# Kernel tuning notes

Measured on AMD Instinct MI355X. Metric: run time of the kernel, lower is better.

## Reference

```python
import jax, jax.numpy as jnp
import numpy as np

D_MODEL = 256
N_HEADS = 8
D_K = D_MODEL // N_HEADS
FFN_DIM = 1024
LN_EPS = 1e-5


def _layernorm(x, g, b):
    mu = jnp.mean(x, axis=-1, keepdims=True)
    var = jnp.var(x, axis=-1, keepdims=True)
    return (x - mu) * jax.lax.rsqrt(var + LN_EPS) * g + b


def setup_inputs() -> dict:
    key = jax.random.key(0)
    ks = jax.random.split(key, 16)
    B, Q, K = 2, 2048, 64
    s = 1.0 / np.sqrt(D_MODEL)
    inp = {
        "target_queries": jax.random.normal(ks[0], (B, Q, D_MODEL), jnp.float32),
        "sampled_features": jax.random.normal(ks[1], (B, Q, K, D_MODEL), jnp.float32),
        "Wq": jax.random.normal(ks[2], (D_MODEL, D_MODEL), jnp.float32) * s,
        "bq": jnp.zeros((D_MODEL,), jnp.float32),
        "Wk": jax.random.normal(ks[3], (D_MODEL, D_MODEL), jnp.float32) * s,
        "bk": jnp.zeros((D_MODEL,), jnp.float32),
        "Wv": jax.random.normal(ks[4], (D_MODEL, D_MODEL), jnp.float32) * s,
        "bv": jnp.zeros((D_MODEL,), jnp.float32),
        "Wo": jax.random.normal(ks[5], (D_MODEL, D_MODEL), jnp.float32) * s,
        "bo": jnp.zeros((D_MODEL,), jnp.float32),
        "g1": jnp.ones((D_MODEL,), jnp.float32),
        "beta1": jnp.zeros((D_MODEL,), jnp.float32),
        "g2": jnp.ones((D_MODEL,), jnp.float32),
        "beta2": jnp.zeros((D_MODEL,), jnp.float32),
        "W1": jax.random.normal(ks[6], (D_MODEL, FFN_DIM), jnp.float32) * s,
        "b1": jnp.zeros((FFN_DIM,), jnp.float32),
        "W2": jax.random.normal(ks[7], (FFN_DIM, D_MODEL), jnp.float32) * (1.0 / np.sqrt(FFN_DIM)),
        "b2": jnp.zeros((D_MODEL,), jnp.float32),
    }
    return inp


def reference(target_queries, sampled_features, Wq, bq, Wk, bk, Wv, bv, Wo, bo,
              g1, beta1, g2, beta2, W1, b1, W2, b2):
    B, Q, C = target_queries.shape
    K = sampled_features.shape[2]
    H, Dk = N_HEADS, D_K

    # pre-norm + projections (dropout is identity at eval)
    qn = _layernorm(target_queries, g1, beta1)
    q = (qn @ Wq + bq).reshape(B, Q, H, Dk).transpose(0, 2, 1, 3)            # bhqd
    k = (sampled_features @ Wk + bk).reshape(B, Q, K, H, Dk).transpose(0, 3, 1, 2, 4)  # bhqkd
    v = (sampled_features @ Wv + bv).reshape(B, Q, K, H, Dk).transpose(0, 3, 1, 2, 4)  # bhqkd

    # per-query gathered K/V attention
    scores = jnp.einsum('bhqd,bhqkd->bhqk', q, k) / np.sqrt(Dk).astype(np.float32)
    attn_weights = jax.nn.softmax(scores, axis=-1)                            # (B,H,Q,K)
    attn_out = jnp.einsum('bhqk,bhqkd->bhqd', attn_weights, v)
    attn_out = attn_out.transpose(0, 2, 1, 3).reshape(B, Q, C)
    attn_out = attn_out @ Wo + bo

    x = target_queries + attn_out

    # FFN with pre-norm residual (exact erf GELU, as torch default)
    h = _layernorm(x, g2, beta2)
    h = jax.nn.gelu(h @ W1 + b1, approximate=False) @ W2 + b2
    out = x + h
    return out, attn_weights
```

## Files before the change

kernel.cpp:

```cpp
#include <hip/hip_runtime.h>
#include <math.h>

#define QTOT 2048

using bf16x8 = __attribute__((ext_vector_type(8))) short;
using f32x4  = __attribute__((ext_vector_type(4))) float;

static __device__ __forceinline__ short f2bf(float f) {
    union { float f; unsigned u; } v; v.f = f;
    unsigned r = v.u + 0x7fffu + ((v.u >> 16) & 1u);
    return (short)(r >> 16);
}
static __device__ __forceinline__ unsigned cvt_pk(float a, float b) {
    unsigned r;
    asm("v_cvt_pk_bf16_f32 %0, %1, %2" : "=v"(r) : "v"(a), "v"(b));
    return r;
}
static __device__ __forceinline__ bf16x8 pack8(float a0, float a1, float a2, float a3,
                                               float a4, float a5, float a6, float a7) {
    union { unsigned u[4]; bf16x8 v; } z;
    z.u[0] = cvt_pk(a0, a1); z.u[1] = cvt_pk(a2, a3);
    z.u[2] = cvt_pk(a4, a5); z.u[3] = cvt_pk(a6, a7);
    return z.v;
}

__global__ void wconv(const float* __restrict__ Wq, const float* __restrict__ Wk,
                      const float* __restrict__ Wo, const float* __restrict__ Wv,
                      const float* __restrict__ W1, const float* __restrict__ W2,
                      short* __restrict__ WqP, short* __restrict__ WkP,
                      short* __restrict__ WoP, short* __restrict__ WvP,
                      short* __restrict__ W1P, short* __restrict__ W2P) {
    int b = blockIdx.x, t = threadIdx.x;
    const float* W; short* P; int N, KK, ci; bool tr = false;
    if (b < 32)       { W = Wq; P = WqP; N = 256;  KK = 8;  ci = b * 256 + t; }
    else if (b < 64)  { W = Wk; P = WkP; N = 256;  KK = 8;  ci = (b - 32) * 256 + t; tr = true; }
    else if (b < 96)  { W = Wo; P = WoP; N = 256;  KK = 8;  ci = (b - 64) * 256 + t; }
    else if (b < 128) { W = Wv; P = WvP; N = 256;  KK = 8;  ci = (b - 96) * 256 + t; }
    else if (b < 256) { W = W1; P = W1P; N = 1024; KK = 8;  ci = (b - 128) * 256 + t; }
    else              { W = W2; P = W2P; N = 256;  KK = 32; ci = (b - 256) * 256 + t; }
    int cb = ci / (KK * 64);
    int rem = ci - cb * (KK * 64);
    int kk = rem >> 6, l = rem & 63;
    int lr = l & 15, lg = l >> 4;
    int n = cb * 16 + lr, k0 = kk * 32 + lg * 8;
    short pk[8];
    if (!tr) {
#pragma unroll
        for (int e = 0; e < 8; ++e) pk[e] = f2bf(W[(size_t)(k0 + e) * N + n]);
    } else {
#pragma unroll
        for (int e = 0; e < 8; ++e) pk[e] = f2bf(W[(size_t)n * 256 + (k0 + e)]);
    }
    *reinterpret_cast<bf16x8*>(P + (size_t)ci * 8) = *reinterpret_cast<bf16x8*>(pk);
}

__global__ void ln1z(const float* __restrict__ tq, const short* __restrict__ WqP,
                     const float* __restrict__ bq, const float* __restrict__ g1,
                     const float* __restrict__ be1, const short* __restrict__ WkP,
                     const float* __restrict__ bk, short* __restrict__ zf,
                     float* __restrict__ sbg) {
    __shared__ float xs[8 * 260];
    __shared__ float qs[8 * 260];
    __shared__ short zst[8 * 2048];
    int r0 = blockIdx.x * 8, t = threadIdx.x;
    int w = t >> 6, l = t & 63, lr = l & 15, lg = l >> 4;
#pragma unroll
    for (int it = 0; it < 8; ++it) xs[it * 260 + t] = tq[(size_t)(r0 + it) * 256 + t];
    __syncthreads();
#pragma unroll
    for (int i = 0; i < 2; ++i) {
        int r = w * 2 + i;
        float s = 0.f, s2 = 0.f;
        for (int j = l; j < 256; j += 64) { float x = xs[r * 260 + j]; s += x; s2 += x * x; }
#pragma unroll
        for (int m = 1; m < 64; m <<= 1) { s += __shfl_xor(s, m); s2 += __shfl_xor(s2, m); }
        float mu = s * (1.f / 256.f);
        float var = s2 * (1.f / 256.f) - mu * mu;
        float rstd = rsqrtf(var + 1e-5f);
        for (int j = l; j < 256; j += 64)
            xs[r * 260 + j] = (xs[r * 260 + j] - mu) * rstd * g1[j] + be1[j];
    }
    __syncthreads();
    f32x4 cq[4];
#pragma unroll
    for (int ni = 0; ni < 4; ++ni) cq[ni] = (f32x4){0.f, 0.f, 0.f, 0.f};
#pragma unroll
    for (int kk = 0; kk < 8; ++kk) {
        bf16x8 af = {0, 0, 0, 0, 0, 0, 0, 0};
        if (lr < 8) {
            const float* xp = &xs[lr * 260 + kk * 32 + lg * 8];
            af = pack8(xp[0], xp[1], xp[2], xp[3], xp[4], xp[5], xp[6], xp[7]);
        }
#pragma unroll
        for (int ni = 0; ni < 4; ++ni) {
            bf16x8 bf = *reinterpret_cast<const bf16x8*>(WqP + ((size_t)((w * 4 + ni) * 8 + kk) * 64 + l) * 8);
            cq[ni] = __builtin_amdgcn_mfma_f32_16x16x32_bf16(af, bf, cq[ni], 0, 0, 0);
        }
    }
    if (lg < 2) {
#pragma unroll
        for (int ni = 0; ni < 4; ++ni)
#pragma unroll
            for (int r = 0; r < 4; ++r) {
                int row = lg * 4 + r, col = (w * 4 + ni) * 16 + lr;
                qs[row * 260 + col] = cq[ni][r] + bq[col];
            }
    }
    __syncthreads();
    if (t < 64) {
        int r = t >> 3, h = t & 7;
        float s = 0.f;
        for (int d = 0; d < 32; ++d) s += qs[r * 260 + h * 32 + d] * bk[h * 32 + d];
        sbg[(size_t)(r0 + r) * 8 + h] = s;
    }
    f32x4 cz[4][4];
#pragma unroll
    for (int mi = 0; mi < 4; ++mi)
#pragma unroll
        for (int ni = 0; ni < 4; ++ni) cz[mi][ni] = (f32x4){0.f, 0.f, 0.f, 0.f};
#pragma unroll
    for (int kk = 0; kk < 8; ++kk) {
        bf16x8 am[4];
#pragma unroll
        for (int mi = 0; mi < 4; ++mi) {
            bf16x8 z = {0, 0, 0, 0, 0, 0, 0, 0};
            if ((lr & 7) == kk) {
                int rr = mi * 2 + (lr >> 3);
                const float* qp = &qs[rr * 260 + kk * 32 + lg * 8];
                z = pack8(qp[0], qp[1], qp[2], qp[3], qp[4], qp[5], qp[6], qp[7]);
            }
            am[mi] = z;
        }
#pragma unroll
        for (int ni = 0; ni < 4; ++ni) {
            bf16x8 bf = *reinterpret_cast<const bf16x8*>(WkP + ((size_t)((w * 4 + ni) * 8 + kk) * 64 + l) * 8);
#pragma unroll
            for (int mi = 0; mi < 4; ++mi)
                cz[mi][ni] = __builtin_amdgcn_mfma_f32_16x16x32_bf16(am[mi], bf, cz[mi][ni], 0, 0, 0);
        }
    }
#pragma unroll
    for (int mi = 0; mi < 4; ++mi)
#pragma unroll
        for (int ni = 0; ni < 4; ++ni)
#pragma unroll
            for (int r = 0; r < 4; ++r) {
                int mrow = mi * 16 + lg * 4 + r;
                int rr = mrow >> 3, hh = mrow & 7;
                int i = (w * 4 + ni) * 16 + lr;
                zst[rr * 2048 + (i >> 3) * 64 + hh * 8 + (i & 7)] = f2bf(cz[mi][ni][r]);
            }
    __syncthreads();
#pragma unroll
    for (int it = 0; it < 8; ++it) {
        int c = it * 256 + t;
        *reinterpret_cast<bf16x8*>(zf + (size_t)r0 * 2048 + (size_t)c * 8) =
            *reinterpret_cast<const bf16x8*>(&zst[c * 8]);
    }
}

__launch_bounds__(256, 4)
__global__ void attn(const float* __restrict__ sf, const short* __restrict__ zf,
                     const float* __restrict__ sbg, const short* __restrict__ WvP,
                     const float* __restrict__ bv, short* __restrict__ aob,
                     float* __restrict__ attn_w) {
    __shared__ __align__(16) char arena[39040];
    char* Xb = arena;
    float* sp = reinterpret_cast<float*>(arena + 32768);
    char* Ub = arena + 34944;

    int bq = blockIdx.x, t = threadIdx.x;
    int w = t >> 6, l = t & 63, lr = l & 15, lg = l >> 4;
    const float* Xg = sf + (size_t)bq * 16384;

    float4 fa[16];
#pragma unroll
    for (int q = 0; q < 8; ++q) {
        int c = q * 256 + t;
        fa[2 * q]     = *reinterpret_cast<const float4*>(Xg + c * 8);
        fa[2 * q + 1] = *reinterpret_cast<const float4*>(Xg + c * 8 + 4);
    }
    bf16x8 zfr[8];
#pragma unroll
    for (int kk = 0; kk < 8; ++kk) {
        bf16x8 z = {0, 0, 0, 0, 0, 0, 0, 0};
        if (lr < 8)
            z = *reinterpret_cast<const bf16x8*>(zf + (size_t)bq * 2048 + ((size_t)((kk * 4 + lg) * 8 + lr)) * 8);
        zfr[kk] = z;
    }
#pragma unroll
    for (int q = 0; q < 8; ++q) {
        int c = q * 256 + t;
        int key = c >> 5, ch = (c & 31) * 8;
        int base = (key * 512 + ch * 2) ^ ((key & 7) << 4);
        *reinterpret_cast<bf16x8*>(Xb + base) =
            pack8(fa[2 * q].x, fa[2 * q].y, fa[2 * q].z, fa[2 * q].w,
                  fa[2 * q + 1].x, fa[2 * q + 1].y, fa[2 * q + 1].z, fa[2 * q + 1].w);
    }
    __syncthreads();

    f32x4 cs = {0.f, 0.f, 0.f, 0.f};
    {
        int key = w * 16 + lr;
        int swz = (key & 7) << 4;
#pragma unroll
        for (int kk = 0; kk < 8; ++kk) {
            int addr = (key * 512 + kk * 64 + lg * 16) ^ swz;
            bf16x8 xb = *reinterpret_cast<const bf16x8*>(Xb + addr);
            cs = __builtin_amdgcn_mfma_f32_16x16x32_bf16(zfr[kk], xb, cs, 0, 0, 0);
        }
    }
    if (lg < 2) {
#pragma unroll
        for (int r = 0; r < 4; ++r)
            sp[(lg * 4 + r) * 68 + w * 16 + lr] = cs[r];
    }
    __syncthreads();

    const float scale = 0.17677669529663687f;
    int b = bq >> 11, qq = bq & 2047;
#pragma unroll
    for (int hi = 0; hi < 2; ++hi) {
        int h = w * 2 + hi;
        float sbh = sbg[(size_t)bq * 8 + h];
        float s = (sp[h * 68 + l] + sbh) * scale;
        float m = s;
#pragma unroll
        for (int off = 1; off < 64; off <<= 1) m = fmaxf(m, __shfl_xor(m, off));
        float p = __expf(s - m);
        float sm = p;
#pragma unroll
        for (int off = 1; off < 64; off <<= 1) sm += __shfl_xor(sm, off);
        float P = p / sm;
        sp[h * 68 + l] = P;
        attn_w[(((size_t)b * 8 + h) * QTOT + qq) * 64 + l] = P;
    }
    __syncthreads();

    {
        int h = t >> 5, cg = t & 31;
        float acc[8];
#pragma unroll
        for (int e = 0; e < 8; ++e) acc[e] = 0.f;
#pragma unroll
        for (int k4 = 0; k4 < 16; ++k4) {
            float4 pv = *reinterpret_cast<const float4*>(&sp[h * 68 + k4 * 4]);
#pragma unroll
            for (int e = 0; e < 4; ++e) {
                int key = k4 * 4 + e;
                float P = (e == 0) ? pv.x : (e == 1) ? pv.y : (e == 2) ? pv.z : pv.w;
                int addr = (key * 512 + cg * 16) ^ ((key & 7) << 4);
                union { bf16x8 v; unsigned u[4]; } xv;
                xv.v = *reinterpret_cast<const bf16x8*>(Xb + addr);
#pragma unroll
                for (int d = 0; d < 4; ++d) {
                    union { unsigned u; float f; } lo, hi;
                    lo.u = xv.u[d] << 16;
                    hi.u = xv.u[d] & 0xffff0000u;
                    acc[2 * d]     += P * lo.f;
                    acc[2 * d + 1] += P * hi.f;
                }
            }
        }
        int ub = (h * 512 + cg * 16) ^ ((h & 7) << 4);
        *reinterpret_cast<bf16x8*>(Ub + ub) =
            pack8(acc[0], acc[1], acc[2], acc[3], acc[4], acc[5], acc[6], acc[7]);
    }
    __syncthreads();

    f32x4 co[4];
#pragma unroll
    for (int ni = 0; ni < 4; ++ni) co[ni] = (f32x4){0.f, 0.f, 0.f, 0.f};
#pragma unroll
    for (int kk = 0; kk < 8; ++kk) {
        bf16x8 ua = {0, 0, 0, 0, 0, 0, 0, 0};
        if (lr < 8) {
            int addr = (lr * 512 + kk * 64 + lg * 16) ^ ((lr & 7) << 4);
            ua = *reinterpret_cast<const bf16x8*>(Ub + addr);
        }
#pragma unroll
        for (int ni = 0; ni < 4; ++ni) {
            bf16x8 bf = *reinterpret_cast<const bf16x8*>(WvP + ((size_t)((w * 4 + ni) * 8 + kk) * 64 + l) * 8);
            co[ni] = __builtin_amdgcn_mfma_f32_16x16x32_bf16(ua, bf, co[ni], 0, 0, 0);
        }
    }
    if (lg < 2) {
#pragma unroll
        for (int ni = 0; ni < 4; ++ni) {
            int j = (w * 4 + ni) * 16 + lr;
            int h = j >> 5;
            if ((h >> 2) == lg)
                aob[(size_t)bq * 256 + j] = f2bf(co[ni][h & 3] + bv[j]);
        }
    }
}

__launch_bounds__(512, 1)
__global__ void tail(const short* __restrict__ aob, const float* __restrict__ tq,
                     const short* __restrict__ WoP, const float* __restrict__ bo,
                     const float* __restrict__ g2, const float* __restrict__ be2,
                     const short* __restrict__ W1P, const float* __restrict__ b1,
                     const short* __restrict__ W2P, const float* __restrict__ b2,
                     float* __restrict__ out) {
    __shared__ float xrow[16][260];
    __shared__ short xn[16][264];
    __shared__ short hs[16][1048];
    int r0 = blockIdx.x * 16, t = threadIdx.x;
    int w = t >> 6, l = t & 63, lr = l & 15, lg = l >> 4;

    f32x4 c[2];
#pragma unroll
    for (int ni = 0; ni < 2; ++ni) c[ni] = (f32x4){0.f, 0.f, 0.f, 0.f};
#pragma unroll
    for (int kk = 0; kk < 8; ++kk) {
        bf16x8 af = *reinterpret_cast<const bf16x8*>(aob + (size_t)(r0 + lr) * 256 + kk * 32 + lg * 8);
#pragma unroll
        for (int ni = 0; ni < 2; ++ni) {
            bf16x8 bf = *reinterpret_cast<const bf16x8*>(WoP + ((size_t)((w * 2 + ni) * 8 + kk) * 64 + l) * 8);
            c[ni] = __builtin_amdgcn_mfma_f32_16x16x32_bf16(af, bf, c[ni], 0, 0, 0);
        }
    }
#pragma unroll
    for (int ni = 0; ni < 2; ++ni) {
        int col = (w * 2 + ni) * 16 + lr;
        float bb = bo[col];
#pragma unroll
        for (int r = 0; r < 4; ++r) {
            int row = lg * 4 + r;
            xrow[row][col] = tq[(size_t)(r0 + row) * 256 + col] + c[ni][r] + bb;
        }
    }
    __syncthreads();

#pragma unroll
    for (int i = 0; i < 2; ++i) {
        int r = w * 2 + i;
        float s = 0.f, s2 = 0.f;
        for (int j = l; j < 256; j += 64) { float x = xrow[r][j]; s += x; s2 += x * x; }
#pragma unroll
        for (int m = 1; m < 64; m <<= 1) { s += __shfl_xor(s, m); s2 += __shfl_xor(s2, m); }
        float mu = s * (1.f / 256.f);
        float var = s2 * (1.f / 256.f) - mu * mu;
        float rstd = rsqrtf(var + 1e-5f);
        for (int j = l; j < 256; j += 64)
            xn[r][j] = f2bf((xrow[r][j] - mu) * rstd * g2[j] + be2[j]);
    }
    __syncthreads();

    bf16x8 af1[8];
#pragma unroll
    for (int kk = 0; kk < 8; ++kk)
        af1[kk] = *reinterpret_cast<const bf16x8*>(&xn[lr][kk * 32 + lg * 8]);
#pragma unroll
    for (int nt = 0; nt < 8; ++nt) {
        int cb = w * 8 + nt;
        f32x4 cc = {0.f, 0.f, 0.f, 0.f};
#pragma unroll
        for (int kk = 0; kk < 8; ++kk) {
            bf16x8 bf = *reinterpret_cast<const bf16x8*>(W1P + ((size_t)(cb * 8 + kk) * 64 + l) * 8);
            cc = __builtin_amdgcn_mfma_f32_16x16x32_bf16(af1[kk], bf, cc, 0, 0, 0);
        }
        int col = cb * 16 + lr;
        float bb = b1[col];
#pragma unroll
        for (int r = 0; r < 4; ++r) {
            int row = lg * 4 + r;
            float v = cc[r] + bb;
            float g = 0.5f * v * (1.f + erff(v * 0.7071067811865475f));
            hs[row][col] = f2bf(g);
        }
    }
    __syncthreads();

    f32x4 c2[2];
#pragma unroll
    for (int ni = 0; ni < 2; ++ni) c2[ni] = (f32x4){0.f, 0.f, 0.f, 0.f};
#pragma unroll
    for (int kk = 0; kk < 32; ++kk) {
        bf16x8 af = *reinterpret_cast<const bf16x8*>(&hs[lr][kk * 32 + lg * 8]);
#pragma unroll
        for (int ni = 0; ni < 2; ++ni) {
            bf16x8 bf = *reinterpret_cast<const bf16x8*>(W2P + ((size_t)((w * 2 + ni) * 32 + kk) * 64 + l) * 8);
            c2[ni] = __builtin_amdgcn_mfma_f32_16x16x32_bf16(af, bf, c2[ni], 0, 0, 0);
        }
    }
#pragma unroll
    for (int ni = 0; ni < 2; ++ni) {
        int col = (w * 2 + ni) * 16 + lr;
        float bb = b2[col];
#pragma unroll
        for (int r = 0; r < 4; ++r) {
            int row = lg * 4 + r;
            out[(size_t)(r0 + row) * 256 + col] = xrow[row][col] + c2[ni][r] + bb;
        }
    }
}

extern "C" void kernel_launch(void* const* d_in, const int* in_sizes, int n_in,
                              void* d_out, int out_size, void* d_ws, size_t ws_size,
                              hipStream_t stream) {
    const float* tq  = (const float*)d_in[0];
    const float* sf  = (const float*)d_in[1];
    const float* Wq  = (const float*)d_in[2];
    const float* bq  = (const float*)d_in[3];
    const float* Wk  = (const float*)d_in[4];
    const float* bk  = (const float*)d_in[5];
    const float* Wv  = (const float*)d_in[6];
    const float* bv  = (const float*)d_in[7];
    const float* Wo  = (const float*)d_in[8];
    const float* bo  = (const float*)d_in[9];
    const float* g1  = (const float*)d_in[10];
    const float* be1 = (const float*)d_in[11];
    const float* g2  = (const float*)d_in[12];
    const float* be2 = (const float*)d_in[13];
    const float* W1  = (const float*)d_in[14];
    const float* b1  = (const float*)d_in[15];
    const float* W2  = (const float*)d_in[16];
    const float* b2  = (const float*)d_in[17];

    char* wsb = (char*)d_ws;
    short* WqP = (short*)(wsb + 0);
    short* WkP = (short*)(wsb + 131072);
    short* WoP = (short*)(wsb + 262144);
    short* WvP = (short*)(wsb + 393216);
    short* W1P = (short*)(wsb + 524288);
    short* W2P = (short*)(wsb + 1048576);
    float* sbw = (float*)(wsb + 1572864);
    short* zf  = (short*)(wsb + 1703936);
    short* aob = (short*)(wsb + 18481152);

    float* outp   = (float*)d_out;
    float* attnwp = (float*)d_out + 1048576;

    wconv<<<384, 256, 0, stream>>>(Wq, Wk, Wo, Wv, W1, W2, WqP, WkP, WoP, WvP, W1P, W2P);
    ln1z<<<512, 256, 0, stream>>>(tq, WqP, bq, g1, be1, WkP, bk, zf, sbw);
    attn<<<4096, 256, 0, stream>>>(sf, zf, sbw, WvP, bv, aob, attnwp);
    tail<<<256, 512, 0, stream>>>(aob, tq, WoP, bo, g2, be2, W1P, b1, W2P, b2, outp);
}
```

Baseline: 130.5 us.

## Fold Wv into Wo as per-head fused matrix and move V projection to tail

Precomputes a per-head fused Wv·Wo weight (2048x256 in bf16) and a fused bias bv·Wo+bo in the weight-conversion kernel. The attention kernel now writes only the per-head attention-weighted raw features (2048 values per query), with no V projection MFMAs, their LDS buffer or two barriers. The tail kernel's output projection becomes a K=2048 GEMM over these features. This removes per-block V-projection work and weight reloads in attn, but adds 8x more intermediate global traffic and a larger GEMM in tail, which runs with only 256 blocks.

```diff
diff --git a/kernel.cpp b/kernel.cpp
--- a/kernel.cpp
+++ b/kernel.cpp
@@ -25,33 +25,90 @@
 }
 
 __global__ void wconv(const float* __restrict__ Wq, const float* __restrict__ Wk,
-                      const float* __restrict__ Wo, const float* __restrict__ Wv,
+                      const float* __restrict__ Wv, const float* __restrict__ Wo,
                       const float* __restrict__ W1, const float* __restrict__ W2,
+                      const float* __restrict__ bv, const float* __restrict__ bo,
                       short* __restrict__ WqP, short* __restrict__ WkP,
-                      short* __restrict__ WoP, short* __restrict__ WvP,
-                      short* __restrict__ W1P, short* __restrict__ W2P) {
+                      short* __restrict__ W1P, short* __restrict__ W2P,
+                      short* __restrict__ WvoP, float* __restrict__ bop) {
+    __shared__ short zb[32 * 256];
     int b = blockIdx.x, t = threadIdx.x;
-    const float* W; short* P; int N, KK, ci; bool tr = false;
-    if (b < 32)       { W = Wq; P = WqP; N = 256;  KK = 8;  ci = b * 256 + t; }
-    else if (b < 64)  { W = Wk; P = WkP; N = 256;  KK = 8;  ci = (b - 32) * 256 + t; tr = true; }
-    else if (b < 96)  { W = Wo; P = WoP; N = 256;  KK = 8;  ci = (b - 64) * 256 + t; }
-    else if (b < 128) { W = Wv; P = WvP; N = 256;  KK = 8;  ci = (b - 96) * 256 + t; }
-    else if (b < 256) { W = W1; P = W1P; N = 1024; KK = 8;  ci = (b - 128) * 256 + t; }
-    else              { W = W2; P = W2P; N = 256;  KK = 32; ci = (b - 256) * 256 + t; }
-    int cb = ci / (KK * 64);
-    int rem = ci - cb * (KK * 64);
-    int kk = rem >> 6, l = rem & 63;
-    int lr = l & 15, lg = l >> 4;
-    int n = cb * 16 + lr, k0 = kk * 32 + lg * 8;
-    short pk[8];
-    if (!tr) {
-#pragma unroll
-        for (int e = 0; e < 8; ++e) pk[e] = f2bf(W[(size_t)(k0 + e) * N + n]);
-    } else {
-#pragma unroll
-        for (int e = 0; e < 8; ++e) pk[e] = f2bf(W[(size_t)n * 256 + (k0 + e)]);
-    }
-    *reinterpret_cast<bf16x8*>(P + (size_t)ci * 8) = *reinterpret_cast<bf16x8*>(pk);
+    if (b < 320) {
+        const float* W; short* P; int N, KK, ci; bool tr = false;
+        if (b < 32)       { W = Wq; P = WqP; N = 256;  KK = 8;  ci = b * 256 + t; }
+        else if (b < 64)  { W = Wk; P = WkP; N = 256;  KK = 8;  ci = (b - 32) * 256 + t; tr = true; }
+        else if (b < 192) { W = W1; P = W1P; N = 1024; KK = 8;  ci = (b - 64) * 256 + t; }
+        else              { W = W2; P = W2P; N = 256;  KK = 32; ci = (b - 192) * 256 + t; }
+        int cb = ci / (KK * 64);
+        int rem = ci - cb * (KK * 64);
+        int kk = rem >> 6, l = rem & 63;
+        int lr = l & 15, lg = l >> 4;
+        int n = cb * 16 + lr, k0 = kk * 32 + lg * 8;
+        short pk[8];
+        if (!tr) {
+#pragma unroll
+            for (int e = 0; e < 8; ++e) pk[e] = f2bf(W[(size_t)(k0 + e) * N + n]);
+        } else {
+#pragma unroll
+            for (int e = 0; e < 8; ++e) pk[e] = f2bf(W[(size_t)n * 256 + (k0 + e)]);
+        }
+        *reinterpret_cast<bf16x8*>(P + (size_t)ci * 8) = *reinterpret_cast<bf16x8*>(pk);
+        return;
+    }
+    if (b == 384) {
+        float s = bo[t];
+        for (int j = 0; j < 256; ++j) s += bv[j] * Wo[(size_t)j * 256 + t];
+        bop[t] = s;
+        return;
+    }
+    int hb = b - 320;
+    int h = hb >> 3, ct = hb & 7;
+    int kko = h * 8 + ct;
+    int w = t >> 6, l = t & 63, lr = l & 15, lg = l >> 4;
+    bf16x8 am[2];
+#pragma unroll
+    for (int mi = 0; mi < 2; ++mi) {
+        int cc = ct * 32 + mi * 16 + lr;
+        const float* ap = Wv + (size_t)cc * 256 + h * 32 + lg * 8;
+        float4 a0 = *reinterpret_cast<const float4*>(ap);
+        float4 a1 = *reinterpret_cast<const float4*>(ap + 4);
+        am[mi] = pack8(a0.x, a0.y, a0.z, a0.w, a1.x, a1.y, a1.z, a1.w);
+    }
+    f32x4 c[2][4];
+#pragma unroll
+    for (int mi = 0; mi < 2; ++mi)
+#pragma unroll
+        for (int ni = 0; ni < 4; ++ni) c[mi][ni] = (f32x4){0.f, 0.f, 0.f, 0.f};
+#pragma unroll
+    for (int ni = 0; ni < 4; ++ni) {
+        int n = (w * 4 + ni) * 16 + lr;
+        short pk[8];
+#pragma unroll
+        for (int e = 0; e < 8; ++e)
+            pk[e] = f2bf(Wo[(size_t)(h * 32 + lg * 8 + e) * 256 + n]);
+        bf16x8 bfr = *reinterpret_cast<bf16x8*>(pk);
+#pragma unroll
+        for (int mi = 0; mi < 2; ++mi)
+            c[mi][ni] = __builtin_amdgcn_mfma_f32_16x16x32_bf16(am[mi], bfr, c[mi][ni], 0, 0, 0);
+    }
+#pragma unroll
+    for (int mi = 0; mi < 2; ++mi)
+#pragma unroll
+        for (int ni = 0; ni < 4; ++ni)
+#pragma unroll
+            for (int r = 0; r < 4; ++r)
+                zb[(mi * 16 + lg * 4 + r) * 256 + (w * 4 + ni) * 16 + lr] = f2bf(c[mi][ni][r]);
+    __syncthreads();
+#pragma unroll
+    for (int it = 0; it < 4; ++it) {
+        int idx = it * 256 + t;
+        int cb = idx >> 6, l2 = idx & 63, lr2 = l2 & 15, lg2 = l2 >> 4;
+        short pk[8];
+#pragma unroll
+        for (int e = 0; e < 8; ++e) pk[e] = zb[(lg2 * 8 + e) * 256 + cb * 16 + lr2];
+        *reinterpret_cast<bf16x8*>(WvoP + ((size_t)(cb * 64 + kko) * 64 + l2) * 8) =
+            *reinterpret_cast<bf16x8*>(pk);
+    }
 }
 
 __global__ void ln1z(const float* __restrict__ tq, const short* __restrict__ WqP,
@@ -161,13 +218,11 @@
 
 __launch_bounds__(256, 4)
 __global__ void attn(const float* __restrict__ sf, const short* __restrict__ zf,
-                     const float* __restrict__ sbg, const short* __restrict__ WvP,
-                     const float* __restrict__ bv, short* __restrict__ aob,
+                     const float* __restrict__ sbg, short* __restrict__ uout,
                      float* __restrict__ attn_w) {
-    __shared__ __align__(16) char arena[39040];
+    __shared__ __align__(16) char arena[34944];
     char* Xb = arena;
     float* sp = reinterpret_cast<float*>(arena + 32768);
-    char* Ub = arena + 34944;
 
     int bq = blockIdx.x, t = threadIdx.x;
     int w = t >> 6, l = t & 63, lr = l & 15, lg = l >> 4;
@@ -235,7 +290,6 @@
         sp[h * 68 + l] = P;
         attn_w[(((size_t)b * 8 + h) * QTOT + qq) * 64 + l] = P;
     }
-    __syncthreads();
 
     {
         int h = t >> 5, cg = t & 31;
@@ -262,42 +316,14 @@
                 }
             }
         }
-        int ub = (h * 512 + cg * 16) ^ ((h & 7) << 4);
-        *reinterpret_cast<bf16x8*>(Ub + ub) =
+        *reinterpret_cast<bf16x8*>(uout + (size_t)bq * 2048 + (size_t)t * 8) =
             pack8(acc[0], acc[1], acc[2], acc[3], acc[4], acc[5], acc[6], acc[7]);
     }
-    __syncthreads();
-
-    f32x4 co[4];
-#pragma unroll
-    for (int ni = 0; ni < 4; ++ni) co[ni] = (f32x4){0.f, 0.f, 0.f, 0.f};
-#pragma unroll
-    for (int kk = 0; kk < 8; ++kk) {
-        bf16x8 ua = {0, 0, 0, 0, 0, 0, 0, 0};
-        if (lr < 8) {
-            int addr = (lr * 512 + kk * 64 + lg * 16) ^ ((lr & 7) << 4);
-            ua = *reinterpret_cast<const bf16x8*>(Ub + addr);
-        }
-#pragma unroll
-        for (int ni = 0; ni < 4; ++ni) {
-            bf16x8 bf = *reinterpret_cast<const bf16x8*>(WvP + ((size_t)((w * 4 + ni) * 8 + kk) * 64 + l) * 8);
-            co[ni] = __builtin_amdgcn_mfma_f32_16x16x32_bf16(ua, bf, co[ni], 0, 0, 0);
-        }
-    }
-    if (lg < 2) {
-#pragma unroll
-        for (int ni = 0; ni < 4; ++ni) {
-            int j = (w * 4 + ni) * 16 + lr;
-            int h = j >> 5;
-            if ((h >> 2) == lg)
-                aob[(size_t)bq * 256 + j] = f2bf(co[ni][h & 3] + bv[j]);
-        }
-    }
 }
 
 __launch_bounds__(512, 1)
-__global__ void tail(const short* __restrict__ aob, const float* __restrict__ tq,
-                     const short* __restrict__ WoP, const float* __restrict__ bo,
+__global__ void tail(const short* __restrict__ up, const float* __restrict__ tq,
+                     const short* __restrict__ WvoP, const float* __restrict__ bop,
                      const float* __restrict__ g2, const float* __restrict__ be2,
                      const short* __restrict__ W1P, const float* __restrict__ b1,
                      const short* __restrict__ W2P, const float* __restrict__ b2,
@@ -311,19 +337,19 @@
     f32x4 c[2];
 #pragma unroll
     for (int ni = 0; ni < 2; ++ni) c[ni] = (f32x4){0.f, 0.f, 0.f, 0.f};
-#pragma unroll
-    for (int kk = 0; kk < 8; ++kk) {
-        bf16x8 af = *reinterpret_cast<const bf16x8*>(aob + (size_t)(r0 + lr) * 256 + kk * 32 + lg * 8);
+#pragma unroll 8
+    for (int kk = 0; kk < 64; ++kk) {
+        bf16x8 af = *reinterpret_cast<const bf16x8*>(up + (size_t)(r0 + lr) * 2048 + kk * 32 + lg * 8);
 #pragma unroll
         for (int ni = 0; ni < 2; ++ni) {
-            bf16x8 bf = *reinterpret_cast<const bf16x8*>(WoP + ((size_t)((w * 2 + ni) * 8 + kk) * 64 + l) * 8);
+            bf16x8 bf = *reinterpret_cast<const bf16x8*>(WvoP + ((size_t)((w * 2 + ni) * 64 + kk) * 64 + l) * 8);
             c[ni] = __builtin_amdgcn_mfma_f32_16x16x32_bf16(af, bf, c[ni], 0, 0, 0);
         }
     }
 #pragma unroll
     for (int ni = 0; ni < 2; ++ni) {
         int col = (w * 2 + ni) * 16 + lr;
-        float bb = bo[col];
+        float bb = bop[col];
 #pragma unroll
         for (int r = 0; r < 4; ++r) {
             int row = lg * 4 + r;
@@ -419,21 +445,22 @@
     const float* b2  = (const float*)d_in[17];
 
     char* wsb = (char*)d_ws;
-    short* WqP = (short*)(wsb + 0);
-    short* WkP = (short*)(wsb + 131072);
-    short* WoP = (short*)(wsb + 262144);
-    short* WvP = (short*)(wsb + 393216);
-    short* W1P = (short*)(wsb + 524288);
-    short* W2P = (short*)(wsb + 1048576);
-    float* sbw = (float*)(wsb + 1572864);
-    short* zf  = (short*)(wsb + 1703936);
-    short* aob = (short*)(wsb + 18481152);
+    short* WqP  = (short*)(wsb + 0);
+    short* WkP  = (short*)(wsb + 131072);
+    short* W1P  = (short*)(wsb + 262144);
+    short* W2P  = (short*)(wsb + 786432);
+    short* WvoP = (short*)(wsb + 1310720);
+    float* bop  = (float*)(wsb + 2359296);
+    float* sbw  = (float*)(wsb + 2360320);
+    short* zf   = (short*)(wsb + 2491392);
+    short* uws  = (short*)(wsb + 19268608);
 
     float* outp   = (float*)d_out;
     float* attnwp = (float*)d_out + 1048576;
 
-    wconv<<<384, 256, 0, stream>>>(Wq, Wk, Wo, Wv, W1, W2, WqP, WkP, WoP, WvP, W1P, W2P);
+    wconv<<<385, 256, 0, stream>>>(Wq, Wk, Wv, Wo, W1, W2, bv, bo,
+                                   WqP, WkP, W1P, W2P, WvoP, bop);
     ln1z<<<512, 256, 0, stream>>>(tq, WqP, bq, g1, be1, WkP, bk, zf, sbw);
-    attn<<<4096, 256, 0, stream>>>(sf, zf, sbw, WvP, bv, aob, attnwp);
-    tail<<<256, 512, 0, stream>>>(aob, tq, WoP, bo, g2, be2, W1P, b1, W2P, b2, outp);
-}
+    attn<<<4096, 256, 0, stream>>>(sf, zf, sbw, uws, attnwp);
+    tail<<<256, 512, 0, stream>>>(uws, tq, WvoP, bop, g2, be2, W1P, b1, W2P, b2, outp);
+}
```

New measurement: 207.4 us. +58.9%, slower.
